# Performance work log

Hardware: AMD Instinct MI355X
Metric: run time of the kernel (lower is better)

The kernel has to match this reference:

```python
import jax, jax.numpy as jnp
import numpy as np

N, S, EMBED, LATENT, HVGS, E = 8192, 128, 256, 128, 2000, 131072


def setup_inputs() -> dict:
    key = jax.random.key(0)
    ks = jax.random.split(key, 12)
    sd = lambda fan_in: 1.0 / np.sqrt(fan_in)
    inp = {
        "emb": jax.random.normal(ks[0], (N, S, EMBED), dtype=jnp.float32),
        "edge_index": jax.random.randint(ks[1], (2, E), 0, N, dtype=jnp.int64),
        "Wq": jax.random.uniform(ks[2], (EMBED, LATENT), jnp.float32, -sd(EMBED), sd(EMBED)),
        "bq": jnp.zeros((LATENT,), jnp.float32),
        "Wk": jax.random.uniform(ks[3], (EMBED, LATENT), jnp.float32, -sd(EMBED), sd(EMBED)),
        "bk": jnp.zeros((LATENT,), jnp.float32),
        "Wv": jax.random.uniform(ks[4], (EMBED, LATENT), jnp.float32, -sd(EMBED), sd(EMBED)),
        "bv": jnp.zeros((LATENT,), jnp.float32),
        "Wo": jax.random.uniform(ks[5], (LATENT, LATENT), jnp.float32, -sd(LATENT), sd(LATENT)),
        "bo": jnp.zeros((LATENT,), jnp.float32),
        "Wg": jax.random.uniform(ks[6], (LATENT, HVGS), jnp.float32, -sd(LATENT), sd(LATENT)),
        "bg": jnp.zeros((HVGS,), jnp.float32),
    }
    return inp


def _gcn(x, W, b, edge_index):
    # PyG GCNConv with add_self_loops=True, symmetric normalization
    h = x @ W  # [N, HVGS]
    n = x.shape[0]
    loop = jnp.arange(n, dtype=edge_index.dtype)
    src = jnp.concatenate([edge_index[0], loop])
    dst = jnp.concatenate([edge_index[1], loop])
    deg = jax.ops.segment_sum(jnp.ones_like(src, dtype=h.dtype), dst, num_segments=n)
    dinv = jnp.where(deg > 0, jax.lax.rsqrt(deg), 0.0)
    norm = dinv[src] * dinv[dst]  # [E+N]
    out = jax.ops.segment_sum(h[src] * norm[:, None], dst, num_segments=n)
    return out + b


def reference(emb, edge_index, Wq, bq, Wk, bk, Wv, bv, Wo, bo, Wg, bg):
    Q = emb @ Wq + bq  # [N, S, L]
    K = emb @ Wk + bk
    V = emb @ Wv + bv
    scale = 1.0 / np.sqrt(emb.shape[-1])
    att_weights = jnp.tanh(jnp.einsum("nsl,ntl->nst", Q, K) * scale)  # [N, S, S]
    att_out = jnp.einsum("nst,ntl->nsl", att_weights, V)
    z = (att_out @ Wo + bo).mean(axis=1)  # [N, L]
    output = _gcn(z, Wg, bg, edge_index)  # [N, HVGS]
    return (att_weights, z, output)
```

## Files before the change

kernel.cpp:

```cpp
#include <hip/hip_runtime.h>
#include <cstdint>
#include <cstddef>

#define NN   8192
#define SS   128
#define EMBD 256
#define LL   128
#define HV   2000
#define EE   131072

typedef float  f32x4  __attribute__((ext_vector_type(4)));
typedef __bf16 bf16x8 __attribute__((ext_vector_type(8)));
typedef unsigned int   u32x4 __attribute__((ext_vector_type(4)));
typedef unsigned short u16x4 __attribute__((ext_vector_type(4)));

__device__ __forceinline__ unsigned short f2bf(float f) {
  unsigned u; __builtin_memcpy(&u, &f, 4);
  unsigned r = u + 0x7fffu + ((u >> 16) & 1u);
  return (unsigned short)(r >> 16);
}
__device__ __forceinline__ float bfLo(unsigned w) {
  unsigned x = w << 16; float f; __builtin_memcpy(&f, &x, 4); return f;
}
__device__ __forceinline__ float bfHi(unsigned w) {
  unsigned x = w & 0xffff0000u; float f; __builtin_memcpy(&f, &x, 4); return f;
}

__global__ void prep_w(const float* __restrict__ Wq, const float* __restrict__ Wk,
                       const float* __restrict__ Wv, unsigned short* __restrict__ wT) {
  int idx = blockIdx.x * 256 + threadIdx.x;
  int c = idx >> 8, e = idx & 255;
  float v = (c < 128) ? Wq[(size_t)e * LL + c]
          : (c < 256) ? Wk[(size_t)e * LL + (c - 128)]
                      : Wv[(size_t)e * LL + (c - 256)];
  wT[idx] = f2bf(v);
}

#define QA_LDS 81920
__global__ __launch_bounds__(512, 2)
void qkatt(const float* __restrict__ emb, const unsigned short* __restrict__ wT,
           const float* __restrict__ bq, const float* __restrict__ bk,
           float* __restrict__ attOut, float* __restrict__ cOut,
           unsigned short* __restrict__ Vout)
{
  extern __shared__ char lds[];
  unsigned short* sE   = (unsigned short*)lds;
  unsigned short* auxV = (unsigned short*)(lds + 65536);
  float* scr = (float*)(lds + 65536);

  const int n    = blockIdx.x;
  const int tid  = threadIdx.x;
  const int wid  = tid >> 6;
  const int lane = tid & 63;
  const int lx   = lane & 15;
  const int g    = lane >> 4;
  const int sw   = (lx & 7) << 3;

  const float* embN = emb + (size_t)n * (SS * EMBD);

  {
    const f32x4* src = (const f32x4*)embN;
    #pragma unroll
    for (int it = 0; it < 16; it++) {
      int i = it * 512 + tid;
      f32x4 v = src[i];
      int s = i >> 6, e0 = (i & 63) << 2;
      u16x4 h;
      h[0] = f2bf(v[0]); h[1] = f2bf(v[1]); h[2] = f2bf(v[2]); h[3] = f2bf(v[3]);
      *(u16x4*)(sE + s * 256 + (e0 ^ ((s & 7) << 3))) = h;
    }
  }
  __syncthreads();

  const int col0 = (wid << 5) + lx;
  const int vcol = (wid << 4) + lx;
  float bias[2];
  bias[0] = (col0      < 128) ? bq[col0]      : bk[col0 - 128];
  bias[1] = (col0 + 16 < 128) ? bq[col0 + 16] : bk[col0 + 16 - 128];

  #pragma unroll 1
  for (int half = 0; half < 2; half++) {
    {
      f32x4 accV[4];
      #pragma unroll
      for (int m = 0; m < 4; m++) accV[m] = f32x4{0.f, 0.f, 0.f, 0.f};
      u32x4 B[8];
      const unsigned short* wp = wT + (size_t)(256 + vcol) * 256 + g * 8;
      #pragma unroll
      for (int ks = 0; ks < 8; ks++) B[ks] = *(const u32x4*)(wp + ks * 32);
      #pragma unroll
      for (int m = 0; m < 4; m++) {
        const unsigned short* ap = sE + (half * 64 + m * 16 + lx) * 256;
        #pragma unroll
        for (int ks = 0; ks < 8; ks++) {
          u32x4 A = *(const u32x4*)(ap + ((ks * 32 + g * 8) ^ sw));
          accV[m] = __builtin_amdgcn_mfma_f32_16x16x32_bf16(
                      __builtin_bit_cast(bf16x8, A), __builtin_bit_cast(bf16x8, B[ks]),
                      accV[m], 0, 0, 0);
        }
      }
      #pragma unroll
      for (int m = 0; m < 4; m++)
        #pragma unroll
        for (int r = 0; r < 4; r++)
          auxV[(m * 16 + g * 4 + r) * 128 + vcol] = f2bf(accV[m][r]);
    }

    f32x4 acc[2][4];
    #pragma unroll
    for (int n2 = 0; n2 < 2; n2++)
      #pragma unroll
      for (int m = 0; m < 4; m++) acc[n2][m] = f32x4{0.f, 0.f, 0.f, 0.f};

    #pragma unroll
    for (int n2 = 0; n2 < 2; n2++) {
      u32x4 B[8];
      const unsigned short* wp = wT + (size_t)(col0 + n2 * 16) * 256 + g * 8;
      #pragma unroll
      for (int ks = 0; ks < 8; ks++) B[ks] = *(const u32x4*)(wp + ks * 32);
      #pragma unroll
      for (int m = 0; m < 4; m++) {
        const unsigned short* ap = sE + (half * 64 + m * 16 + lx) * 256;
        #pragma unroll
        for (int ks = 0; ks < 8; ks++) {
          u32x4 A = *(const u32x4*)(ap + ((ks * 32 + g * 8) ^ sw));
          acc[n2][m] = __builtin_amdgcn_mfma_f32_16x16x32_bf16(
                         __builtin_bit_cast(bf16x8, A), __builtin_bit_cast(bf16x8, B[ks]),
                         acc[n2][m], 0, 0, 0);
        }
      }
    }
    __syncthreads();

    #pragma unroll
    for (int n2 = 0; n2 < 2; n2++) {
      const int col = col0 + n2 * 16;
      const float bb = bias[n2];
      #pragma unroll
      for (int m = 0; m < 4; m++)
        #pragma unroll
        for (int r = 0; r < 4; r++) {
          const int srow = half * 64 + m * 16 + g * 4 + r;
          sE[srow * 256 + (col ^ ((srow & 7) << 3))] = f2bf(acc[n2][m][r] + bb);
        }
    }
    {
      const u32x4* s4 = (const u32x4*)auxV;
      u32x4* dst = (u32x4*)(Vout + ((size_t)n * 128 + half * 64) * 128);
      dst[tid]       = s4[tid];
      dst[512 + tid] = s4[512 + tid];
    }
    __syncthreads();
  }

  bf16x8 qf[4];
  #pragma unroll
  for (int ks = 0; ks < 4; ks++)
    qf[ks] = __builtin_bit_cast(bf16x8,
      *(const u32x4*)(sE + (wid * 16 + lx) * 256 + ((ks * 32 + g * 8) ^ sw)));

  f32x4 accS[8];
  #pragma unroll
  for (int nt = 0; nt < 8; nt++) accS[nt] = f32x4{0.f, 0.f, 0.f, 0.f};
  #pragma unroll
  for (int nt = 0; nt < 8; nt++) {
    const int tr = nt * 16 + lx;
    #pragma unroll
    for (int ks = 0; ks < 4; ks++) {
      u32x4 t = *(const u32x4*)(sE + tr * 256 + 128 + ((ks * 32 + g * 8) ^ sw));
      accS[nt] = __builtin_amdgcn_mfma_f32_16x16x32_bf16(
                   qf[ks], __builtin_bit_cast(bf16x8, t), accS[nt], 0, 0, 0);
    }
  }

  {
    float* slot = attOut + (size_t)n * (SS * SS);
    const int srow0 = wid * 16 + g * 4;
    float colp[8];
    #pragma unroll
    for (int nt = 0; nt < 8; nt++) {
      float p = 0.f;
      #pragma unroll
      for (int r = 0; r < 4; r++) {
        float x  = accS[nt][r] * 0.0625f;
        float ax = fabsf(x);
        float ex = __expf(ax * 2.0f);
        float th = __builtin_copysignf(__fdividef(ex - 1.0f, ex + 1.0f), x);
        p += th;
        slot[(size_t)(srow0 + r) * SS + nt * 16 + lx] = th;
      }
      p += __shfl_xor(p, 16, 64);
      p += __shfl_xor(p, 32, 64);
      colp[nt] = p;
    }
    if (lane < 16) {
      #pragma unroll
      for (int nt = 0; nt < 8; nt++) scr[wid * 128 + nt * 16 + lane] = colp[nt];
    }
  }
  __syncthreads();

  if (tid < 128) {
    float s = 0.f;
    #pragma unroll
    for (int w = 0; w < 8; w++) s += scr[w * 128 + tid];
    cOut[(size_t)n * 128 + tid] = s * (1.0f / 128.0f);
  }
}

__global__ __launch_bounds__(256)
void zkerV(const unsigned short* __restrict__ V, const float* __restrict__ cIn,
           const float* __restrict__ bv, const float* __restrict__ Wo,
           const float* __restrict__ bo, float* __restrict__ zOut)
{
  __shared__ float cS[128], mS[128], scrV[512], scr2[256], csS[2];
  const int n = blockIdx.x, tid = threadIdx.x;

  if (tid < 128) {
    float c = cIn[(size_t)n * 128 + tid];
    cS[tid] = c;
    float r = c;
    #pragma unroll
    for (int off = 32; off >= 1; off >>= 1) r += __shfl_down(r, off, 64);
    if ((tid & 63) == 0) csS[tid >> 6] = r;
  }
  __syncthreads();

  {
    const int cp = tid & 63, tg = tid >> 6;
    const unsigned* vp = (const unsigned*)(V + (size_t)n * (128 * 128)) + cp;
    float a0 = 0.f, a1 = 0.f;
    #pragma unroll 4
    for (int t = tg; t < 128; t += 4) {
      unsigned w = vp[(size_t)t * 64];
      a0 += cS[t] * bfLo(w);
      a1 += cS[t] * bfHi(w);
    }
    scrV[tg * 128 + cp * 2]     = a0;
    scrV[tg * 128 + cp * 2 + 1] = a1;
  }
  __syncthreads();
  if (tid < 128) {
    float csum = csS[0] + csS[1];
    mS[tid] = scrV[tid] + scrV[128 + tid] + scrV[256 + tid] + scrV[384 + tid]
            + csum * bv[tid];
  }
  __syncthreads();

  {
    const int j = tid & 127, h = tid >> 7;
    float a = 0.f;
    #pragma unroll 8
    for (int i = 0; i < 64; i++)
      a += mS[h * 64 + i] * Wo[(size_t)(h * 64 + i) * LL + j];
    scr2[tid] = a;
  }
  __syncthreads();
  if (tid < 128)
    zOut[(size_t)n * LL + tid] = scr2[tid] + scr2[128 + tid] + bo[tid];
}

__global__ void gcn_deg(const int* __restrict__ eidx, float* __restrict__ deg) {
  int e = blockIdx.x * 256 + threadIdx.x;
  if (e < EE) atomicAdd(&deg[eidx[EE + e]], 1.0f);
}

__global__ void gcn_dinv(const float* __restrict__ deg, float* __restrict__ dinv) {
  int i = blockIdx.x * 256 + threadIdx.x;
  if (i < NN) dinv[i] = rsqrtf(deg[i] + 1.0f);
}

__global__ void gcn_self(const float* __restrict__ dinv, const float* __restrict__ z,
                         float* __restrict__ agg) {
  size_t gidx = (size_t)blockIdx.x * 256 + threadIdx.x;
  int i = (int)(gidx >> 7);
  float di = dinv[i];
  agg[gidx] = di * di * z[gidx];
}

__global__ void gcn_scatter(const int* __restrict__ eidx, const float* __restrict__ dinv,
                            const float* __restrict__ z, float* __restrict__ agg) {
  int w    = (blockIdx.x * blockDim.x + threadIdx.x) >> 6;
  int lane = threadIdx.x & 63;
  int nw   = (gridDim.x * blockDim.x) >> 6;
  for (int e = w; e < EE; e += nw) {
    int s = eidx[e], d = eidx[EE + e];
    float nrm = dinv[s] * dinv[d];
    atomicAdd(&agg[(size_t)d * 128 + lane],      nrm * z[(size_t)s * 128 + lane]);
    atomicAdd(&agg[(size_t)d * 128 + 64 + lane], nrm * z[(size_t)s * 128 + 64 + lane]);
  }
}

__global__ __launch_bounds__(256)
void out_gemm(const float* __restrict__ agg, const float* __restrict__ Wg,
              const float* __restrict__ bg, float* __restrict__ outp) {
  __shared__ float sA[8 * 128];
  const int nb = blockIdx.x * 8;
  const int tid = threadIdx.x;
  {
    const float4* src = (const float4*)(agg + (size_t)nb * 128);
    ((float4*)sA)[tid] = src[tid];
  }
  __syncthreads();
  const int g0 = tid * 8;
  if (g0 < HV) {
    float acc[8][8];
    #pragma unroll
    for (int i = 0; i < 8; i++)
      #pragma unroll
      for (int j = 0; j < 8; j++) acc[i][j] = 0.0f;
    #pragma unroll 2
    for (int l = 0; l < 128; l++) {
      float4 wa = *(const float4*)(Wg + (size_t)l * HV + g0);
      float4 wb = *(const float4*)(Wg + (size_t)l * HV + g0 + 4);
      float w[8] = {wa.x, wa.y, wa.z, wa.w, wb.x, wb.y, wb.z, wb.w};
      #pragma unroll
      for (int i = 0; i < 8; i++) {
        float a = sA[i * 128 + l];
        #pragma unroll
        for (int j = 0; j < 8; j++) acc[i][j] += a * w[j];
      }
    }
    float b[8];
    #pragma unroll
    for (int j = 0; j < 8; j++) b[j] = bg[g0 + j];
    #pragma unroll
    for (int i = 0; i < 8; i++) {
      float4 oa = make_float4(acc[i][0] + b[0], acc[i][1] + b[1], acc[i][2] + b[2], acc[i][3] + b[3]);
      float4 ob = make_float4(acc[i][4] + b[4], acc[i][5] + b[5], acc[i][6] + b[6], acc[i][7] + b[7]);
      *(float4*)(outp + (size_t)(nb + i) * HV + g0)     = oa;
      *(float4*)(outp + (size_t)(nb + i) * HV + g0 + 4) = ob;
    }
  }
}

extern "C" void kernel_launch(void* const* d_in, const int* in_sizes, int n_in,
                              void* d_out, int out_size, void* d_ws, size_t ws_size,
                              hipStream_t stream) {
  const float* emb  = (const float*)d_in[0];
  const int*   eidx = (const int*)d_in[1];
  const float* Wq = (const float*)d_in[2];
  const float* bq = (const float*)d_in[3];
  const float* Wk = (const float*)d_in[4];
  const float* bk = (const float*)d_in[5];
  const float* Wv = (const float*)d_in[6];
  const float* bv = (const float*)d_in[7];
  const float* Wo = (const float*)d_in[8];
  const float* bo = (const float*)d_in[9];
  const float* Wg = (const float*)d_in[10];
  const float* bg = (const float*)d_in[11];

  float* out  = (float*)d_out;
  float* attO = out;
  float* zO   = out + (size_t)NN * SS * SS;
  float* oO   = zO + (size_t)NN * LL;

  float* wsf  = (float*)d_ws;
  float* deg  = wsf;
  float* dinv = wsf + NN;
  float* agg  = wsf + 2 * NN;
  unsigned short* wT = (unsigned short*)(wsf + 2 * NN + (size_t)NN * 128);
  float* cWS  = (float*)((char*)wT + 3 * LL * EMBD * sizeof(unsigned short));
  unsigned short* Vws = (unsigned short*)(cWS + (size_t)NN * 128);

  (void)in_sizes; (void)n_in; (void)out_size; (void)ws_size;

  hipFuncSetAttribute((const void*)qkatt,
                      hipFuncAttributeMaxDynamicSharedMemorySize, QA_LDS);

  hipMemsetAsync(deg, 0, NN * sizeof(float), stream);
  gcn_deg <<<EE / 256, 256, 0, stream>>>(eidx, deg);
  gcn_dinv<<<NN / 256, 256, 0, stream>>>(deg, dinv);
  prep_w  <<<(3 * LL * EMBD) / 256, 256, 0, stream>>>(Wq, Wk, Wv, wT);

  qkatt<<<NN, 512, QA_LDS, stream>>>(emb, wT, bq, bk, attO, cWS, Vws);
  zkerV<<<NN, 256, 0, stream>>>(Vws, cWS, bv, Wo, bo, zO);

  gcn_self   <<<NN * 128 / 256, 256, 0, stream>>>(dinv, zO, agg);
  gcn_scatter<<<2048, 256, 0, stream>>>(eidx, dinv, zO, agg);
  out_gemm   <<<NN / 8, 256, 0, stream>>>(agg, Wg, bg, oO);
}
```

Before: 869.2 us.

## Write V transposed from registers, drop LDS staging, and raise qkatt occupancy

The qkatt kernel now writes the V projection straight from the MFMA accumulators to global memory in a column-major, pair-packed bf16 layout. This removes the 16KB LDS staging buffer, which cuts the kernel's LDS request and lets the launch bound ask for 4 blocks per CU instead of 2. zkerV then loads the transposed V tile into padded LDS and does its weighted sum over rows per column from there. The costs are scattered 8-byte global stores instead of coalesced 16-byte ones, plus possible register pressure under the tighter launch bound.

```diff
diff --git a/kernel.cpp b/kernel.cpp
--- a/kernel.cpp
+++ b/kernel.cpp
@@ -12,6 +12,7 @@
 typedef float  f32x4  __attribute__((ext_vector_type(4)));
 typedef __bf16 bf16x8 __attribute__((ext_vector_type(8)));
 typedef unsigned int   u32x4 __attribute__((ext_vector_type(4)));
+typedef unsigned int   u32x2 __attribute__((ext_vector_type(2)));
 typedef unsigned short u16x4 __attribute__((ext_vector_type(4)));
 
 __device__ __forceinline__ unsigned short f2bf(float f) {
@@ -36,16 +37,15 @@
   wT[idx] = f2bf(v);
 }
 
-#define QA_LDS 81920
-__global__ __launch_bounds__(512, 2)
+#define QA_LDS (65536 + 4096)
+__global__ __launch_bounds__(512, 4)
 void qkatt(const float* __restrict__ emb, const unsigned short* __restrict__ wT,
            const float* __restrict__ bq, const float* __restrict__ bk,
            float* __restrict__ attOut, float* __restrict__ cOut,
-           unsigned short* __restrict__ Vout)
+           unsigned* __restrict__ Vt)
 {
   extern __shared__ char lds[];
-  unsigned short* sE   = (unsigned short*)lds;
-  unsigned short* auxV = (unsigned short*)(lds + 65536);
+  unsigned short* sE = (unsigned short*)lds;
   float* scr = (float*)(lds + 65536);
 
   const int n    = blockIdx.x;
@@ -99,11 +99,15 @@
                       accV[m], 0, 0, 0);
         }
       }
-      #pragma unroll
-      for (int m = 0; m < 4; m++)
-        #pragma unroll
-        for (int r = 0; r < 4; r++)
-          auxV[(m * 16 + g * 4 + r) * 128 + vcol] = f2bf(accV[m][r]);
+      unsigned* vdst = Vt + (size_t)n * (128 * 64) + (size_t)vcol * 64
+                     + half * 32 + g * 2;
+      #pragma unroll
+      for (int m = 0; m < 4; m++) {
+        u32x2 pk;
+        pk[0] = (unsigned)f2bf(accV[m][0]) | ((unsigned)f2bf(accV[m][1]) << 16);
+        pk[1] = (unsigned)f2bf(accV[m][2]) | ((unsigned)f2bf(accV[m][3]) << 16);
+        *(u32x2*)(vdst + m * 8) = pk;
+      }
     }
 
     f32x4 acc[2][4];
@@ -144,12 +148,6 @@
           sE[srow * 256 + (col ^ ((srow & 7) << 3))] = f2bf(acc[n2][m][r] + bb);
         }
     }
-    {
-      const u32x4* s4 = (const u32x4*)auxV;
-      u32x4* dst = (u32x4*)(Vout + ((size_t)n * 128 + half * 64) * 128);
-      dst[tid]       = s4[tid];
-      dst[512 + tid] = s4[512 + tid];
-    }
     __syncthreads();
   }
 
@@ -209,11 +207,12 @@
 }
 
 __global__ __launch_bounds__(256)
-void zkerV(const unsigned short* __restrict__ V, const float* __restrict__ cIn,
+void zkerV(const unsigned* __restrict__ Vt, const float* __restrict__ cIn,
            const float* __restrict__ bv, const float* __restrict__ Wo,
            const float* __restrict__ bo, float* __restrict__ zOut)
 {
-  __shared__ float cS[128], mS[128], scrV[512], scr2[256], csS[2];
+  __shared__ unsigned sV[128 * 65];
+  __shared__ float cS[128], mS[128], scr2[256], csS[2];
   const int n = blockIdx.x, tid = threadIdx.x;
 
   if (tid < 128) {
@@ -224,26 +223,35 @@
     for (int off = 32; off >= 1; off >>= 1) r += __shfl_down(r, off, 64);
     if ((tid & 63) == 0) csS[tid >> 6] = r;
   }
-  __syncthreads();
-
-  {
-    const int cp = tid & 63, tg = tid >> 6;
-    const unsigned* vp = (const unsigned*)(V + (size_t)n * (128 * 128)) + cp;
-    float a0 = 0.f, a1 = 0.f;
-    #pragma unroll 4
-    for (int t = tg; t < 128; t += 4) {
-      unsigned w = vp[(size_t)t * 64];
-      a0 += cS[t] * bfLo(w);
-      a1 += cS[t] * bfHi(w);
-    }
-    scrV[tg * 128 + cp * 2]     = a0;
-    scrV[tg * 128 + cp * 2 + 1] = a1;
+
+  {
+    const u32x4* src = (const u32x4*)(Vt + (size_t)n * (128 * 64));
+    #pragma unroll
+    for (int it = 0; it < 8; it++) {
+      int i = it * 256 + tid;
+      u32x4 v = src[i];
+      int col = i >> 4, rp0 = (i & 15) << 2;
+      unsigned* d = sV + col * 65 + rp0;
+      d[0] = v[0]; d[1] = v[1]; d[2] = v[2]; d[3] = v[3];
+    }
+  }
+  __syncthreads();
+
+  {
+    const int l = tid & 127, h = tid >> 7;
+    const unsigned* vp = sV + l * 65;
+    float a = 0.f;
+    #pragma unroll 8
+    for (int rp = h * 32; rp < h * 32 + 32; rp++) {
+      unsigned w = vp[rp];
+      a += cS[2 * rp] * bfLo(w) + cS[2 * rp + 1] * bfHi(w);
+    }
+    scr2[tid] = a;
   }
   __syncthreads();
   if (tid < 128) {
     float csum = csS[0] + csS[1];
-    mS[tid] = scrV[tid] + scrV[128 + tid] + scrV[256 + tid] + scrV[384 + tid]
-            + csum * bv[tid];
+    mS[tid] = scr2[tid] + scr2[128 + tid] + csum * bv[tid];
   }
   __syncthreads();
 
@@ -361,7 +369,7 @@
   float* agg  = wsf + 2 * NN;
   unsigned short* wT = (unsigned short*)(wsf + 2 * NN + (size_t)NN * 128);
   float* cWS  = (float*)((char*)wT + 3 * LL * EMBD * sizeof(unsigned short));
-  unsigned short* Vws = (unsigned short*)(cWS + (size_t)NN * 128);
+  unsigned* Vws = (unsigned*)(cWS + (size_t)NN * 128);
 
   (void)in_sizes; (void)n_in; (void)out_size; (void)ws_size;
 
```

Result: slower. 1.307 ms (+50.4%).
